# Optimization experiments

Hardware: AMD Instinct MI355X
Metric: run time of the kernel (lower is better)

The kernel has to match this reference:

```python
import jax, jax.numpy as jnp
import numpy as np

# ---- static config (mirrors MonitorRetina init) ----
N, S, H, W = 256, 1, 144, 256        # stimulus: [N, S, H, W]
HR, WR = 144, 256                    # retina height/width
FOV_HALF_RAD = 0.5 * 75.0 * np.pi / 180.0   # Angular retina, degrees=75
GELU_GAMMA = 1.7015043497085571      # variance-preserving gain for gelu
OUT_OF_RANGE = 10.0                  # grid value for rays missing the monitor


def isotropic_grid_2d(h, w):
    """Pixel-center coordinates, isotropic (normalized by max dim), [-1,1] on the long axis."""
    m = float(max(h, w))
    y = (jnp.arange(h, dtype=jnp.float32) * 2.0 + 1.0 - h) / m
    x = (jnp.arange(w, dtype=jnp.float32) * 2.0 + 1.0 - w) / m
    gy, gx = jnp.meshgrid(y, x, indexing="ij")
    return gx, gy  # each [h, w]


def rmat_3d(ax, ay, az):
    """Batched 3D rotation matrix R = Rz @ Ry @ Rx from Euler angles, each [N]."""
    cx, sx = jnp.cos(ax), jnp.sin(ax)
    cy, sy = jnp.cos(ay), jnp.sin(ay)
    cz, sz = jnp.cos(az), jnp.sin(az)
    one, zero = jnp.ones_like(ax), jnp.zeros_like(ax)
    Rx = jnp.stack([one, zero, zero, zero, cx, -sx, zero, sx, cx], -1).reshape(-1, 3, 3)
    Ry = jnp.stack([cy, zero, sy, zero, one, zero, -sy, zero, cy], -1).reshape(-1, 3, 3)
    Rz = jnp.stack([cz, -sz, zero, sz, cz, zero, zero, zero, one], -1).reshape(-1, 3, 3)
    return jnp.einsum("nij,njk,nkl->nil", Rz, Ry, Rx)  # [N,3,3]


def retina_rays(rmat):
    """Angular retina: pixel angles -> unit ray directions, rotated per batch. [N,HR,WR,3]."""
    gx, gy = isotropic_grid_2d(HR, WR)
    ax, ay = gx * FOV_HALF_RAD, gy * FOV_HALF_RAD
    a = jnp.sqrt(ax * ax + ay * ay) + 1e-12
    sinc = jnp.sin(a) / a
    d = jnp.stack([sinc * ax, sinc * ay, jnp.cos(a)], -1)  # [HR,WR,3]
    return jnp.einsum("nij,hwj->nhwi", rmat, d)


def monitor_project(rays):
    """Plane monitor at unit distance along +z: perspective divide to isotropic grid coords. [N,HR,WR,2]."""
    rz = rays[..., 2]
    safe = rz > 1e-3
    inv = jnp.where(safe, rz, 1.0)
    gx = jnp.where(safe, rays[..., 0] / inv, OUT_OF_RANGE)
    gy = jnp.where(safe, rays[..., 1] / inv, OUT_OF_RANGE)
    return jnp.stack([gx, gy], -1)


def isotropic_grid_sample_2d(x, grid, pad_value=0.0):
    """Bilinear sample x:[N,C,H,W] at grid:[N,H',W',2] (isotropic coords), constant padding."""
    m = float(max(H, W))
    px = (grid[..., 0] * m + W - 1.0) * 0.5  # [N,H',W'] pixel coords
    py = (grid[..., 1] * m + H - 1.0) * 0.5
    x0 = jnp.floor(px)
    y0 = jnp.floor(py)
    wx = px - x0
    wy = py - y0
    x0i = x0.astype(jnp.int32)
    y0i = y0.astype(jnp.int32)

    def corner(img, yi, xi):
        valid = (xi >= 0) & (xi < W) & (yi >= 0) & (yi < H)
        v = img[:, jnp.clip(yi, 0, H - 1), jnp.clip(xi, 0, W - 1)]  # [C,H',W']
        return jnp.where(valid[None], v, pad_value)

    def one(img, y0i, x0i, wx, wy):
        v00 = corner(img, y0i, x0i)
        v01 = corner(img, y0i, x0i + 1)
        v10 = corner(img, y0i + 1, x0i)
        v11 = corner(img, y0i + 1, x0i + 1)
        return (v00 * (1 - wx) + v01 * wx) * (1 - wy) + (v10 * (1 - wx) + v11 * wx) * wy

    return jax.vmap(one)(x, y0i, x0i, wx, wy)  # [N,C,H',W']


def setup_inputs() -> dict:
    key = jax.random.key(0)
    ks = jax.random.split(key, 8)
    F, D = 16, 128
    return {
        "stimulus": jax.random.normal(ks[0], (N, S, H, W), jnp.float32),
        "perspective": jax.random.normal(ks[1], (N, F), jnp.float32),
        "W1": jax.random.normal(ks[2], (F, D), jnp.float32) / np.sqrt(F),
        "b1": jnp.zeros((D,), jnp.float32),
        "W2": jax.random.normal(ks[3], (D, D), jnp.float32) / np.sqrt(D),
        "b2": jnp.zeros((D,), jnp.float32),
        "Wp": jax.random.normal(ks[4], (D, 3), jnp.float32) * 0.05,  # proj gains init near 0
        "bp": jnp.zeros((3,), jnp.float32),
    }


def reference(stimulus, perspective, W1, b1, W2, b2, Wp, bp):
    # MLP -> 3 angles -> rotation matrix (rmat)
    h = jax.nn.gelu(perspective @ W1 + b1) * GELU_GAMMA
    h = jax.nn.gelu(h @ W2 + b2) * GELU_GAMMA
    ang = h @ Wp + bp                      # [N,3]
    rm = rmat_3d(ang[:, 0], ang[:, 1], ang[:, 2])
    rays = retina_rays(rm)                 # [N,HR,WR,3]
    grid = monitor_project(rays)           # [N,HR,WR,2]
    # monitor_pixel / retina_pixel are Raw (identity) transforms
    return isotropic_grid_sample_2d(stimulus, grid, pad_value=0.0)  # [N,S,HR,WR]
```

## Files before the change

kernel.cpp:

```cpp
#include <hip/hip_runtime.h>
#include <math.h>

#define NB    256
#define IMG_H 144
#define IMG_W 256
#define IMG_ELEMS (IMG_H * IMG_W)
#define FDIM  16
#define DDIM  128

#define LDS_STRIDE_H 264
#define LDS_ROWS     (IMG_H + 3)
#define BORDER_CELLS (3 * LDS_STRIDE_H + IMG_H * 8)

#define FOV_HALF_RAD 0.6544984694978736f
#define GELU_GAMMA   1.7015043497085571f
#define OUT_OF_RANGE 10.0f

typedef float    f32x4 __attribute__((ext_vector_type(4)));
typedef _Float16 f16x4 __attribute__((ext_vector_type(4)));
typedef _Float16 f16x2 __attribute__((ext_vector_type(2)));

__device__ __forceinline__ float gelu_gamma(float x) {
    const float k0 = 0.7978845608028654f;
    const float k1 = 0.044715f;
    float t = tanhf(k0 * (x + k1 * x * x * x));
    return 0.5f * x * (1.0f + t) * GELU_GAMMA;
}

__global__ void __launch_bounds__(DDIM) mlp_rmat_kernel(
    const float* __restrict__ persp,
    const float* __restrict__ W1,
    const float* __restrict__ b1,
    const float* __restrict__ W2,
    const float* __restrict__ b2,
    const float* __restrict__ Wp,
    const float* __restrict__ bp,
    float* __restrict__ Rout)
{
    const int n = blockIdx.x;
    const int d = threadIdx.x;

    __shared__ float sh1[DDIM];
    __shared__ float sh2[DDIM];
    __shared__ float ang[3];

    float acc = b1[d];
#pragma unroll
    for (int f = 0; f < FDIM; ++f)
        acc += persp[n * FDIM + f] * W1[f * DDIM + d];
    sh1[d] = gelu_gamma(acc);
    __syncthreads();

    float acc2 = b2[d];
#pragma unroll 8
    for (int k = 0; k < DDIM; ++k)
        acc2 += sh1[k] * W2[k * DDIM + d];
    sh2[d] = gelu_gamma(acc2);
    __syncthreads();

    if (d < 3) {
        float a = bp[d];
#pragma unroll 8
        for (int k = 0; k < DDIM; ++k)
            a += sh2[k] * Wp[k * 3 + d];
        ang[d] = a;
    }
    __syncthreads();

    if (d == 0) {
        float cx = cosf(ang[0]), sx = sinf(ang[0]);
        float cy = cosf(ang[1]), sy = sinf(ang[1]);
        float cz = cosf(ang[2]), sz = sinf(ang[2]);
        float* R = Rout + n * 9;
        R[0] = cz * cy;  R[1] = cz * sy * sx - sz * cx;  R[2] = cz * sy * cx + sz * sx;
        R[3] = sz * cy;  R[4] = sz * sy * sx + cz * cx;  R[5] = sz * sy * cx - cz * sx;
        R[6] = -sy;      R[7] = cy * sx;                 R[8] = cy * cx;
    }
}

__global__ void __launch_bounds__(1024, 8) retina_sample_kernel(
    const float* __restrict__ stim,
    const float* __restrict__ Rmat,
    float* __restrict__ out)
{
    __shared__ __align__(16) _Float16 simg[LDS_ROWS * LDS_STRIDE_H];

    const int tid  = threadIdx.x;
    const int n    = blockIdx.x;
    const int half = blockIdx.y;

    const float* Rn = Rmat + n * 9;
    const float r0 = Rn[0], r1 = Rn[1], r2 = Rn[2];
    const float r3 = Rn[3], r4 = Rn[4], r5 = Rn[5];
    const float r6 = Rn[6], r7 = Rn[7], r8 = Rn[8];

    const float* __restrict__ img = stim + (size_t)n * IMG_ELEMS;

    for (int i = tid; i < BORDER_CELLS; i += 1024) {
        int idx;
        if (i < 3 * LDS_STRIDE_H) {
            const int r3_ = i / LDS_STRIDE_H;
            const int c   = i - r3_ * LDS_STRIDE_H;
            const int r   = (r3_ == 0) ? 0 : (IMG_H + r3_);
            idx = r * LDS_STRIDE_H + c;
        } else {
            const int j = i - 3 * LDS_STRIDE_H;
            const int r = 1 + (j >> 3);
            int c = j & 7;
            c = (c < 4) ? c : (c + 256);
            idx = r * LDS_STRIDE_H + c;
        }
        simg[idx] = (_Float16)0.0f;
    }

    {
        const f32x4* __restrict__ src = (const f32x4*)img;
#pragma unroll
        for (int p = 0; p < 9; ++p) {
            const int g   = tid + p * 1024;
            const int row = g >> 6;
            const int c4  = g & 63;
            const f16x4 hv = __builtin_convertvector(src[g], f16x4);
            *(f16x4*)&simg[(row + 1) * LDS_STRIDE_H + 4 + c4 * 4] = hv;
        }
    }
    __syncthreads();

    const unsigned* __restrict__ U = (const unsigned*)simg;

#pragma unroll
    for (int p = 0; p < 5; ++p) {
        const int gg = p * 1024 + tid;
        if (gg >= 4608) break;
        const int px0 = half * 18432 + gg * 4;
        const int h   = px0 >> 8;
        const int w0  = px0 & 255;

        const float gy  = (2.0f * h + 1.0f - 144.0f) * (1.0f / 256.0f);
        const float ayv = gy * FOV_HALF_RAD;
        const float ay2 = ayv * ayv;
        const float bx = ayv * r1, by = ayv * r4, bz = ayv * r7;

        float wx_[4], wy_[4];
        int dA[4];
        unsigned sh_[4];

#pragma unroll
        for (int j = 0; j < 4; ++j) {
            const float ax = fmaf((float)(w0 + j),
                                  2.0f * FOV_HALF_RAD * (1.0f / 256.0f),
                                  -255.0f * FOV_HALF_RAD * (1.0f / 256.0f));
            const float t = fmaf(ax, ax, ay2);

            float sc = fmaf(t, 2.7557319e-6f, -1.9841270e-4f);
            sc = fmaf(t, sc,  8.3333333e-3f);
            sc = fmaf(t, sc, -1.6666667e-1f);
            sc = fmaf(t, sc,  1.0f);

            float ca = fmaf(t, 2.4801587e-5f, -1.3888889e-3f);
            ca = fmaf(t, ca,  4.1666667e-2f);
            ca = fmaf(t, ca, -0.5f);
            ca = fmaf(t, ca,  1.0f);

            const float rx = fmaf(ca, r2, sc * fmaf(ax, r0, bx));
            const float ry = fmaf(ca, r5, sc * fmaf(ax, r3, by));
            const float rz = fmaf(ca, r8, sc * fmaf(ax, r6, bz));

            const float inv = __builtin_amdgcn_rcpf(rz);
            const bool safe = rz > 0.001f;
            const float gxp = safe ? rx * inv : OUT_OF_RANGE;
            const float gyp = safe ? ry * inv : OUT_OF_RANGE;

            const float pxs = __builtin_amdgcn_fmed3f(
                fmaf(gxp, 128.0f, 128.5f), 0.0f, 257.0f);
            const float pys = __builtin_amdgcn_fmed3f(
                fmaf(gyp, 128.0f, 72.5f), 0.0f, 145.0f);

            const int x0s = (int)pxs;
            const int y0s = (int)pys;
            wx_[j] = pxs - (float)x0s;
            wy_[j] = pys - (float)y0s;

            const int a00 = y0s * LDS_STRIDE_H + x0s + 3;
            dA[j]  = a00 >> 1;
            sh_[j] = (unsigned)(a00 & 1) << 4;
        }

        unsigned u[16];
#pragma unroll
        for (int j = 0; j < 4; ++j) {
            u[4*j+0] = U[dA[j]];
            u[4*j+1] = U[dA[j] + 1];
            u[4*j+2] = U[dA[j] + 132];
            u[4*j+3] = U[dA[j] + 133];
        }

        f32x4 res;
#pragma unroll
        for (int j = 0; j < 4; ++j) {
            const unsigned long long t0 =
                ((unsigned long long)u[4*j+1] << 32) | u[4*j+0];
            const unsigned long long t1 =
                ((unsigned long long)u[4*j+3] << 32) | u[4*j+2];
            const f16x2 h0 = __builtin_bit_cast(f16x2, (unsigned)(t0 >> sh_[j]));
            const f16x2 h1 = __builtin_bit_cast(f16x2, (unsigned)(t1 >> sh_[j]));
            const float v00 = (float)h0[0], v01 = (float)h0[1];
            const float v10 = (float)h1[0], v11 = (float)h1[1];
            const float top = fmaf(wx_[j], v01 - v00, v00);
            const float bot = fmaf(wx_[j], v11 - v10, v10);
            res[j] = fmaf(wy_[j], bot - top, top);
        }

        f32x4* dst = (f32x4*)(out + (size_t)n * IMG_ELEMS + px0);
        __builtin_nontemporal_store(res, dst);
    }
}

extern "C" void kernel_launch(void* const* d_in, const int* in_sizes, int n_in,
                              void* d_out, int out_size, void* d_ws, size_t ws_size,
                              hipStream_t stream) {
    const float* stimulus    = (const float*)d_in[0];
    const float* perspective = (const float*)d_in[1];
    const float* W1          = (const float*)d_in[2];
    const float* b1          = (const float*)d_in[3];
    const float* W2          = (const float*)d_in[4];
    const float* b2          = (const float*)d_in[5];
    const float* Wp          = (const float*)d_in[6];
    const float* bp          = (const float*)d_in[7];
    float* out = (float*)d_out;

    float* Rmat = (float*)d_ws;

    mlp_rmat_kernel<<<NB, DDIM, 0, stream>>>(
        perspective, W1, b1, W2, b2, Wp, bp, Rmat);

    dim3 grid(NB, 2);
    retina_sample_kernel<<<grid, 1024, 0, stream>>>(stimulus, Rmat, out);
}
```

Before: 120.2 us.

## Fuse MLP rotation computation into sampling kernel using one dedicated wavefront

```diff
diff --git a/kernel.cpp b/kernel.cpp
--- a/kernel.cpp
+++ b/kernel.cpp
@@ -27,7 +27,8 @@
     return 0.5f * x * (1.0f + t) * GELU_GAMMA;
 }
 
-__global__ void __launch_bounds__(DDIM) mlp_rmat_kernel(
+__global__ void __launch_bounds__(1024, 8) retina_fused_kernel(
+    const float* __restrict__ stim,
     const float* __restrict__ persp,
     const float* __restrict__ W1,
     const float* __restrict__ b1,
@@ -35,96 +36,97 @@
     const float* __restrict__ b2,
     const float* __restrict__ Wp,
     const float* __restrict__ bp,
-    float* __restrict__ Rout)
-{
-    const int n = blockIdx.x;
-    const int d = threadIdx.x;
-
-    __shared__ float sh1[DDIM];
-    __shared__ float sh2[DDIM];
-    __shared__ float ang[3];
-
-    float acc = b1[d];
-#pragma unroll
-    for (int f = 0; f < FDIM; ++f)
-        acc += persp[n * FDIM + f] * W1[f * DDIM + d];
-    sh1[d] = gelu_gamma(acc);
-    __syncthreads();
-
-    float acc2 = b2[d];
-#pragma unroll 8
-    for (int k = 0; k < DDIM; ++k)
-        acc2 += sh1[k] * W2[k * DDIM + d];
-    sh2[d] = gelu_gamma(acc2);
-    __syncthreads();
-
-    if (d < 3) {
-        float a = bp[d];
-#pragma unroll 8
-        for (int k = 0; k < DDIM; ++k)
-            a += sh2[k] * Wp[k * 3 + d];
-        ang[d] = a;
-    }
-    __syncthreads();
-
-    if (d == 0) {
-        float cx = cosf(ang[0]), sx = sinf(ang[0]);
-        float cy = cosf(ang[1]), sy = sinf(ang[1]);
-        float cz = cosf(ang[2]), sz = sinf(ang[2]);
-        float* R = Rout + n * 9;
-        R[0] = cz * cy;  R[1] = cz * sy * sx - sz * cx;  R[2] = cz * sy * cx + sz * sx;
-        R[3] = sz * cy;  R[4] = sz * sy * sx + cz * cx;  R[5] = sz * sy * cx - cz * sx;
-        R[6] = -sy;      R[7] = cy * sx;                 R[8] = cy * cx;
-    }
-}
-
-__global__ void __launch_bounds__(1024, 8) retina_sample_kernel(
-    const float* __restrict__ stim,
-    const float* __restrict__ Rmat,
     float* __restrict__ out)
 {
     __shared__ __align__(16) _Float16 simg[LDS_ROWS * LDS_STRIDE_H];
+    __shared__ float shml[2 * DDIM + 12];
 
     const int tid  = threadIdx.x;
     const int n    = blockIdx.x;
     const int half = blockIdx.y;
 
-    const float* Rn = Rmat + n * 9;
-    const float r0 = Rn[0], r1 = Rn[1], r2 = Rn[2];
-    const float r3 = Rn[3], r4 = Rn[4], r5 = Rn[5];
-    const float r6 = Rn[6], r7 = Rn[7], r8 = Rn[8];
-
-    const float* __restrict__ img = stim + (size_t)n * IMG_ELEMS;
-
-    for (int i = tid; i < BORDER_CELLS; i += 1024) {
-        int idx;
-        if (i < 3 * LDS_STRIDE_H) {
-            const int r3_ = i / LDS_STRIDE_H;
-            const int c   = i - r3_ * LDS_STRIDE_H;
-            const int r   = (r3_ == 0) ? 0 : (IMG_H + r3_);
-            idx = r * LDS_STRIDE_H + c;
-        } else {
-            const int j = i - 3 * LDS_STRIDE_H;
-            const int r = 1 + (j >> 3);
-            int c = j & 7;
-            c = (c < 4) ? c : (c + 256);
-            idx = r * LDS_STRIDE_H + c;
-        }
-        simg[idx] = (_Float16)0.0f;
-    }
-
-    {
-        const f32x4* __restrict__ src = (const f32x4*)img;
-#pragma unroll
-        for (int p = 0; p < 9; ++p) {
-            const int g   = tid + p * 1024;
-            const int row = g >> 6;
-            const int c4  = g & 63;
-            const f16x4 hv = __builtin_convertvector(src[g], f16x4);
-            *(f16x4*)&simg[(row + 1) * LDS_STRIDE_H + 4 + c4 * 4] = hv;
+    if (tid < 64) {
+        const int l = tid;
+        float a0 = b1[l], a1 = b1[l + 64];
+#pragma unroll
+        for (int f = 0; f < FDIM; ++f) {
+            const float pv = persp[n * FDIM + f];
+            a0 = fmaf(pv, W1[f * DDIM + l], a0);
+            a1 = fmaf(pv, W1[f * DDIM + l + 64], a1);
+        }
+        shml[l]      = gelu_gamma(a0);
+        shml[l + 64] = gelu_gamma(a1);
+        __threadfence_block();
+
+        float c0 = b2[l], c1 = b2[l + 64];
+#pragma unroll 8
+        for (int k = 0; k < DDIM; ++k) {
+            const float hv = shml[k];
+            c0 = fmaf(hv, W2[k * DDIM + l], c0);
+            c1 = fmaf(hv, W2[k * DDIM + l + 64], c1);
+        }
+        shml[DDIM + l]      = gelu_gamma(c0);
+        shml[DDIM + l + 64] = gelu_gamma(c1);
+        __threadfence_block();
+
+        if (l < 3) {
+            float a = bp[l];
+#pragma unroll 8
+            for (int k = 0; k < DDIM; ++k)
+                a = fmaf(shml[DDIM + k], Wp[k * 3 + l], a);
+            shml[2 * DDIM + l] = a;
+        }
+        __threadfence_block();
+
+        if (l == 0) {
+            const float ax_ = shml[2 * DDIM + 0];
+            const float ay_ = shml[2 * DDIM + 1];
+            const float az_ = shml[2 * DDIM + 2];
+            const float cx = cosf(ax_), sx = sinf(ax_);
+            const float cy = cosf(ay_), sy = sinf(ay_);
+            const float cz = cosf(az_), sz = sinf(az_);
+            float* R = &shml[2 * DDIM + 3];
+            R[0] = cz * cy;  R[1] = cz * sy * sx - sz * cx;  R[2] = cz * sy * cx + sz * sx;
+            R[3] = sz * cy;  R[4] = sz * sy * sx + cz * cx;  R[5] = sz * sy * cx - cz * sx;
+            R[6] = -sy;      R[7] = cy * sx;                 R[8] = cy * cx;
+        }
+    } else {
+        const int st = tid - 64;
+
+        for (int i = st; i < BORDER_CELLS; i += 960) {
+            int idx;
+            if (i < 3 * LDS_STRIDE_H) {
+                const int r3_ = i / LDS_STRIDE_H;
+                const int c   = i - r3_ * LDS_STRIDE_H;
+                const int r   = (r3_ == 0) ? 0 : (IMG_H + r3_);
+                idx = r * LDS_STRIDE_H + c;
+            } else {
+                const int j = i - 3 * LDS_STRIDE_H;
+                const int r = 1 + (j >> 3);
+                int c = j & 7;
+                c = (c < 4) ? c : (c + 256);
+                idx = r * LDS_STRIDE_H + c;
+            }
+            simg[idx] = (_Float16)0.0f;
+        }
+
+        const f32x4* __restrict__ src = (const f32x4*)(stim + (size_t)n * IMG_ELEMS);
+#pragma unroll
+        for (int p = 0; p < 10; ++p) {
+            const int g = st + p * 960;
+            if (g < 9216) {
+                const int row = g >> 6;
+                const int c4  = g & 63;
+                const f16x4 hv = __builtin_convertvector(src[g], f16x4);
+                *(f16x4*)&simg[(row + 1) * LDS_STRIDE_H + 4 + c4 * 4] = hv;
+            }
         }
     }
     __syncthreads();
+
+    const float r0 = shml[2 * DDIM + 3 + 0], r1 = shml[2 * DDIM + 3 + 1], r2 = shml[2 * DDIM + 3 + 2];
+    const float r3 = shml[2 * DDIM + 3 + 3], r4 = shml[2 * DDIM + 3 + 4], r5 = shml[2 * DDIM + 3 + 5];
+    const float r6 = shml[2 * DDIM + 3 + 6], r7 = shml[2 * DDIM + 3 + 7], r8 = shml[2 * DDIM + 3 + 8];
 
     const unsigned* __restrict__ U = (const unsigned*)simg;
 
@@ -229,11 +231,7 @@
     const float* bp          = (const float*)d_in[7];
     float* out = (float*)d_out;
 
-    float* Rmat = (float*)d_ws;
-
-    mlp_rmat_kernel<<<NB, DDIM, 0, stream>>>(
-        perspective, W1, b1, W2, b2, Wp, bp, Rmat);
-
     dim3 grid(NB, 2);
-    retina_sample_kernel<<<grid, 1024, 0, stream>>>(stimulus, Rmat, out);
+    retina_fused_kernel<<<grid, 1024, 0, stream>>>(
+        stimulus, perspective, W1, b1, W2, b2, Wp, bp, out);
 }
```

New measurement: 119.3 us. Within noise of the previous version (-0.8%).
